# Performance work log

Hardware: AMD Instinct MI355X
Metric: run time of the kernel (lower is better)

Reference implementation:

```python
import jax, jax.numpy as jnp
import numpy as np

RADIUS = 0.2
NSAMPLE = 32
USE_XYZ = True

B, N, S, C = 8, 8192, 2048, 64


def setup_inputs() -> dict:
    key = jax.random.key(0)
    k1, k2, k3 = jax.random.split(key, 3)
    xyz = jax.random.uniform(k1, (B, N, 3), dtype=jnp.float32)
    new_xyz = jax.random.uniform(k2, (B, S, 3), dtype=jnp.float32)
    features = jax.random.normal(k3, (B, N, C), dtype=jnp.float32)
    return {"xyz": xyz, "new_xyz": new_xyz, "features": features}


def _ball_query(new_xyz, xyz, radius, nsample):
    # new_xyz: (B,S,3), xyz: (B,N,3) -> idx (B,S,nsample) int32
    n = xyz.shape[1]
    d2 = jnp.sum((new_xyz[:, :, None, :] - xyz[:, None, :, :]) ** 2, axis=-1)  # (B,S,N)
    mask = d2 < radius * radius
    # keys: index j if inside ball else N (sentinel); smallest nsample keys = first
    # nsample in-ball indices in ascending j order (matches CUDA ball_query order).
    keys = jnp.where(mask, jnp.arange(n, dtype=jnp.int32), jnp.int32(n))
    neg_vals, _ = jax.lax.top_k(-keys, nsample)  # top_k of -keys -> smallest keys
    idx = -neg_vals  # (B,S,nsample), ascending
    first = idx[..., 0:1]
    idx = jnp.where(idx == n, first, idx)   # pad empty slots with first hit
    idx = jnp.where(idx == n, 0, idx)       # balls with zero hits -> index 0
    return idx


def _group(points, idx):
    # points: (B,N,D), idx: (B,S,K) -> (B,S,K,D)
    return jax.vmap(lambda p, i: p[i])(points, idx)


def reference(xyz, new_xyz, features):
    idx = _ball_query(new_xyz, xyz, RADIUS, NSAMPLE)
    grouped_xyz = _group(xyz, idx) - new_xyz[:, :, None, :]  # (B,S,K,3)
    grouped_feat = _group(features, idx)                      # (B,S,K,C)
    if USE_XYZ:
        new_features = jnp.concatenate([grouped_xyz, grouped_feat], axis=-1)
    else:
        new_features = grouped_feat
    return jnp.transpose(new_features, (0, 3, 1, 2))  # (B, C+3, S, K)
```

## Files before the change

kernel.cpp:

```cpp
#include <hip/hip_runtime.h>

#define BB 8
#define NN 8192
#define SS 2048
#define CC 64
#define NS 32
#define COUT 67
#define QT 8
#define PMAX 35

__global__ __launch_bounds__(256) void scan_kernel(
    const float* __restrict__ xyz,
    const float* __restrict__ new_xyz,
    int* __restrict__ idx_ws)
{
#pragma clang fp contract(off)
    const int wave = threadIdx.x >> 6;
    const int lane = threadIdx.x & 63;
    const int qid  = blockIdx.x * 4 + wave;
    const int b = qid >> 11;
    const int s = qid & 2047;

    const float R2 = 0.04f;

    const float* ctr = new_xyz + ((size_t)b * SS + s) * 3;
    const float cx = ctr[0], cy = ctr[1], cz = ctr[2];
    const float* xb = xyz + (size_t)b * NN * 3;

    int* myidx = idx_ws + (size_t)qid * NS;
    const unsigned long long lt = (1ull << lane) - 1ull;

    int total = 0;
    int firstIdx = -1;
    for (int j0 = 0; j0 < NN && total < NS; j0 += 256) {
        float d2v[4];
#pragma unroll
        for (int u = 0; u < 4; ++u) {
            const int j = j0 + u * 64 + lane;
            const float* p = xb + (size_t)j * 3;
            const float dx = p[0] - cx;
            const float dy = p[1] - cy;
            const float dz = p[2] - cz;
            float d2 = dx * dx;
            d2 = d2 + dy * dy;
            d2 = d2 + dz * dz;
            d2v[u] = d2;
        }
#pragma unroll
        for (int u = 0; u < 4; ++u) {
            const bool hit = d2v[u] < R2;
            const unsigned long long mask = __ballot(hit);
            if (firstIdx < 0 && mask != 0ull)
                firstIdx = j0 + u * 64 + __builtin_ctzll(mask);
            if (hit) {
                const int pos = total + __popcll(mask & lt);
                if (pos < NS) myidx[pos] = j0 + u * 64 + lane;
            }
            total += __popcll(mask);
        }
    }
    if (total < NS) {
        const int fill = (total > 0) ? firstIdx : 0;
        if (lane >= total && lane < NS) myidx[lane] = fill;
    }
}

__global__ __launch_bounds__(256) void gather_kernel(
    const float* __restrict__ xyz,
    const float* __restrict__ new_xyz,
    const float* __restrict__ feat,
    const int* __restrict__ idx_ws,
    float* __restrict__ out)
{
#pragma clang fp contract(off)
    __shared__ float tile[PMAX * QT * NS];
    __shared__ int idx_sh[QT * NS];

    const int t     = threadIdx.x;
    const int sTile = blockIdx.x;
    const int half  = blockIdx.y;
    const int b     = blockIdx.z;

    const int s0 = sTile * QT;
    const int qbase = (b << 11) + s0;

    idx_sh[t] = idx_ws[(size_t)qbase * NS + t];
    __syncthreads();

    const int q = t >> 5;
    const int row = idx_sh[t];

    const float* frow = feat + ((size_t)b * NN + row) * CC + half * 32;
    if (half == 0) {
        const float* ctr = new_xyz + ((size_t)b * SS + s0 + q) * 3;
        const float* p   = xyz + ((size_t)b * NN + row) * 3;
        tile[0 * 256 + t] = p[0] - ctr[0];
        tile[1 * 256 + t] = p[1] - ctr[1];
        tile[2 * 256 + t] = p[2] - ctr[2];
#pragma unroll
        for (int i = 0; i < 8; ++i) {
            const float4 f = *(const float4*)(frow + i * 4);
            tile[(3 + i * 4 + 0) * 256 + t] = f.x;
            tile[(3 + i * 4 + 1) * 256 + t] = f.y;
            tile[(3 + i * 4 + 2) * 256 + t] = f.z;
            tile[(3 + i * 4 + 3) * 256 + t] = f.w;
        }
    } else {
#pragma unroll
        for (int i = 0; i < 8; ++i) {
            const float4 f = *(const float4*)(frow + i * 4);
            tile[(i * 4 + 0) * 256 + t] = f.x;
            tile[(i * 4 + 1) * 256 + t] = f.y;
            tile[(i * 4 + 2) * 256 + t] = f.z;
            tile[(i * 4 + 3) * 256 + t] = f.w;
        }
    }
    __syncthreads();

    const int P     = half ? 32 : PMAX;
    const int cbase = half ? PMAX : 0;
    const int wv = t >> 6;
    const int ln = t & 63;
    const size_t plane = (size_t)SS * NS;
    float* ob = out + (((size_t)b * COUT + cbase) * SS + s0) * NS;
#pragma unroll
    for (int i = 0; i < 9; ++i) {
        const int p = i * 4 + wv;
        if (p < P) {
            const float4 v = *(const float4*)(tile + p * 256 + ln * 4);
            *(float4*)(ob + (size_t)p * plane + ln * 4) = v;
        }
    }
}

extern "C" void kernel_launch(void* const* d_in, const int* in_sizes, int n_in,
                              void* d_out, int out_size, void* d_ws, size_t ws_size,
                              hipStream_t stream) {
    const float* xyz     = (const float*)d_in[0];
    const float* new_xyz = (const float*)d_in[1];
    const float* feat    = (const float*)d_in[2];
    float* out = (float*)d_out;
    int* idx_ws = (int*)d_ws;

    scan_kernel<<<dim3((BB * SS) / 4), dim3(256), 0, stream>>>(xyz, new_xyz, idx_ws);
    gather_kernel<<<dim3(SS / QT, 2, BB), dim3(256), 0, stream>>>(xyz, new_xyz, feat, idx_ws, out);
}
```

Measured before the change: 195.8 us.

## Transpose xyz to SoA and scan two points per lane with float2 loads

Adds a small pre-pass that converts the AoS xyz array into three separate coordinate arrays in workspace. The ball-query scan then loads coalesced float2 vectors and tests two points per lane per step, covering 512 points per iteration with two ballots. This is meant to remove the strided 12-byte AoS loads and raise memory efficiency in the scan. In exchange it adds an extra kernel launch, extra workspace traffic, and a coarser early-exit granularity.

```diff
diff --git a/kernel.cpp b/kernel.cpp
--- a/kernel.cpp
+++ b/kernel.cpp
@@ -9,8 +9,21 @@
 #define QT 8
 #define PMAX 35
 
+__global__ __launch_bounds__(256) void transpose_kernel(
+    const float* __restrict__ xyz,
+    float* __restrict__ xs, float* __restrict__ ys, float* __restrict__ zs)
+{
+    const int t = blockIdx.x * 256 + threadIdx.x;
+    const float* p = xyz + (size_t)t * 3;
+    xs[t] = p[0];
+    ys[t] = p[1];
+    zs[t] = p[2];
+}
+
 __global__ __launch_bounds__(256) void scan_kernel(
-    const float* __restrict__ xyz,
+    const float* __restrict__ xs,
+    const float* __restrict__ ys,
+    const float* __restrict__ zs,
     const float* __restrict__ new_xyz,
     int* __restrict__ idx_ws)
 {
@@ -25,38 +38,61 @@
 
     const float* ctr = new_xyz + ((size_t)b * SS + s) * 3;
     const float cx = ctr[0], cy = ctr[1], cz = ctr[2];
-    const float* xb = xyz + (size_t)b * NN * 3;
+
+    const float2* xb = (const float2*)(xs + (size_t)b * NN);
+    const float2* yb = (const float2*)(ys + (size_t)b * NN);
+    const float2* zb = (const float2*)(zs + (size_t)b * NN);
 
     int* myidx = idx_ws + (size_t)qid * NS;
     const unsigned long long lt = (1ull << lane) - 1ull;
 
     int total = 0;
     int firstIdx = -1;
-    for (int j0 = 0; j0 < NN && total < NS; j0 += 256) {
-        float d2v[4];
+    for (int j0 = 0; j0 < NN && total < NS; j0 += 512) {
+        float2 X[4], Y[4], Z[4];
 #pragma unroll
         for (int u = 0; u < 4; ++u) {
-            const int j = j0 + u * 64 + lane;
-            const float* p = xb + (size_t)j * 3;
-            const float dx = p[0] - cx;
-            const float dy = p[1] - cy;
-            const float dz = p[2] - cz;
-            float d2 = dx * dx;
-            d2 = d2 + dy * dy;
-            d2 = d2 + dz * dz;
-            d2v[u] = d2;
+            const int i2 = (j0 >> 1) + u * 64 + lane;
+            X[u] = xb[i2];
+            Y[u] = yb[i2];
+            Z[u] = zb[i2];
         }
 #pragma unroll
         for (int u = 0; u < 4; ++u) {
-            const bool hit = d2v[u] < R2;
-            const unsigned long long mask = __ballot(hit);
-            if (firstIdx < 0 && mask != 0ull)
-                firstIdx = j0 + u * 64 + __builtin_ctzll(mask);
-            if (hit) {
-                const int pos = total + __popcll(mask & lt);
-                if (pos < NS) myidx[pos] = j0 + u * 64 + lane;
+            const float dx0 = X[u].x - cx, dx1 = X[u].y - cx;
+            const float dy0 = Y[u].x - cy, dy1 = Y[u].y - cy;
+            const float dz0 = Z[u].x - cz, dz1 = Z[u].y - cz;
+            float d20 = dx0 * dx0;
+            float d21 = dx1 * dx1;
+            d20 = d20 + dy0 * dy0;
+            d21 = d21 + dy1 * dy1;
+            d20 = d20 + dz0 * dz0;
+            d21 = d21 + dz1 * dz1;
+            const bool h0 = d20 < R2;
+            const bool h1 = d21 < R2;
+            const unsigned long long lo = __ballot(h0);
+            const unsigned long long hi = __ballot(h1);
+            const int jg = j0 + u * 128;
+            if (firstIdx < 0 && (lo | hi)) {
+                int cand = 0x7fffffff;
+                if (lo) cand = jg + 2 * __builtin_ctzll(lo);
+                if (hi) {
+                    const int c2 = jg + 2 * __builtin_ctzll(hi) + 1;
+                    cand = (c2 < cand) ? c2 : cand;
+                }
+                firstIdx = cand;
             }
-            total += __popcll(mask);
+            const int clo = __popcll(lo & lt);
+            const int chi = __popcll(hi & lt);
+            if (h0) {
+                const int pos = total + clo + chi;
+                if (pos < NS) myidx[pos] = jg + 2 * lane;
+            }
+            if (h1) {
+                const int pos = total + clo + chi + (h0 ? 1 : 0);
+                if (pos < NS) myidx[pos] = jg + 2 * lane + 1;
+            }
+            total += __popcll(lo) + __popcll(hi);
         }
     }
     if (total < NS) {
@@ -140,8 +176,13 @@
     const float* new_xyz = (const float*)d_in[1];
     const float* feat    = (const float*)d_in[2];
     float* out = (float*)d_out;
-    int* idx_ws = (int*)d_ws;
 
-    scan_kernel<<<dim3((BB * SS) / 4), dim3(256), 0, stream>>>(xyz, new_xyz, idx_ws);
+    int*   idx_ws = (int*)d_ws;
+    float* xs = (float*)((char*)d_ws + (size_t)BB * SS * NS * 4);
+    float* ys = xs + (size_t)BB * NN;
+    float* zs = ys + (size_t)BB * NN;
+
+    transpose_kernel<<<dim3(BB * NN / 256), dim3(256), 0, stream>>>(xyz, xs, ys, zs);
+    scan_kernel<<<dim3((BB * SS) / 4), dim3(256), 0, stream>>>(xs, ys, zs, new_xyz, idx_ws);
     gather_kernel<<<dim3(SS / QT, 2, BB), dim3(256), 0, stream>>>(xyz, new_xyz, feat, idx_ws, out);
 }
```

Result: no change. 197.6 us (+0.9%).
